# Kernel optimization log

Hardware: AMD Instinct MI355X
Metric: run time of the kernel (lower is better)

Reference implementation:

```python
import jax, jax.numpy as jnp
import numpy as np

N_RAYS = 32768
N_SAMPLES = 1048576
HID = 64
STEP = 0.0005


def _mlp(x, W1, b1, W2, b2, W3, b3):
    h = jax.nn.relu(x @ W1 + b1)
    h = jax.nn.relu(h @ W2 + b2)
    return h @ W3 + b3


def setup_inputs() -> dict:
    key = jax.random.key(0)
    ks = jax.random.split(key, 12)
    rays_o = jax.random.normal(ks[0], (N_RAYS, 3), jnp.float32)
    rays_d = jax.random.normal(ks[1], (N_RAYS, 3), jnp.float32)
    rays_d = rays_d / jnp.linalg.norm(rays_d, axis=-1, keepdims=True)
    t_starts = jax.random.uniform(ks[2], (N_SAMPLES,), jnp.float32, 0.0, 1.5)
    t_ends = t_starts + STEP
    ray_indices = jnp.sort(jax.random.randint(ks[3], (N_SAMPLES,), 0, N_RAYS, jnp.int32))
    def lin(k, fin, fout):
        return jax.random.normal(k, (fin, fout), jnp.float32) / np.sqrt(fin)
    return {
        'rays_o': rays_o, 'rays_d': rays_d,
        't_starts': t_starts, 't_ends': t_ends,
        'ray_indices': ray_indices,
        'W_d1': lin(ks[4], 3, HID), 'b_d1': jnp.zeros((HID,), jnp.float32),
        'W_d2': lin(ks[5], HID, HID), 'b_d2': jnp.zeros((HID,), jnp.float32),
        'W_d3': lin(ks[6], HID, 1), 'b_d3': jnp.zeros((1,), jnp.float32),
        'W_r1': lin(ks[7], 3, HID), 'b_r1': jnp.zeros((HID,), jnp.float32),
        'W_r2': lin(ks[8], HID, HID), 'b_r2': jnp.zeros((HID,), jnp.float32),
        'W_r3': lin(ks[9], HID, 3), 'b_r3': jnp.zeros((3,), jnp.float32),
    }


def reference(rays_o, rays_d, t_starts, t_ends, ray_indices,
              W_d1, b_d1, W_d2, b_d2, W_d3, b_d3,
              W_r1, b_r1, W_r2, b_r2, W_r3, b_r3):
    n_rays = rays_o.shape[0]
    mid = (t_starts + t_ends) * 0.5                      # [S]
    # gather ray origins/dirs per sample, compute positions
    positions = rays_o[ray_indices] + rays_d[ray_indices] * mid[:, None]  # [S,3]
    # density query (NGP decoder stand-in), softplus activation like trunc_exp family
    sigmas = jax.nn.softplus(_mlp(positions, W_d1, b_d1, W_d2, b_d2, W_d3, b_d3))[:, 0]  # [S]
    # render_weight_from_density: segment-wise exclusive cumsum of sigma*dt
    sigma_dt = sigmas * (t_ends - t_starts)              # [S]
    excl_global = jnp.cumsum(sigma_dt) - sigma_dt        # global exclusive cumsum
    per_ray = jax.ops.segment_sum(sigma_dt, ray_indices, num_segments=n_rays)  # [R]
    ray_excl = jnp.cumsum(per_ray) - per_ray             # exclusive cumsum over rays
    within_excl = excl_global - ray_excl[ray_indices]    # exclusive within each ray
    trans = jnp.exp(-within_excl)                        # transmittance
    alphas = 1.0 - jnp.exp(-sigma_dt)
    weights = trans * alphas
    # accumulate_along_rays (scatter-sum over ray_indices)
    opacities = jax.ops.segment_sum(weights, ray_indices, num_segments=n_rays)[:, None]  # [R,1]
    distances = jax.ops.segment_sum(weights * mid, ray_indices, num_segments=n_rays)[:, None]
    # rgb query
    rgbs = jax.nn.sigmoid(_mlp(positions, W_r1, b_r1, W_r2, b_r2, W_r3, b_r3))  # [S,3]
    w_sg = jax.lax.stop_gradient(weights)
    colors = jax.ops.segment_sum(w_sg[:, None] * rgbs, ray_indices, num_segments=n_rays)  # [R,3]
    # eval-mode background composition (nerf.training == False branch)
    rest = jax.lax.stop_gradient(1.0 - opacities)
    distances = distances + 5.0 * rest
    colors = colors + 0.5 * rest
    return colors, distances, opacities
```

## Files before the change

### kernel.cpp

```cpp
#include <hip/hip_runtime.h>
#include <hip/hip_bf16.h>
#include <math.h>

#define N_RAYS   32768
#define N_SAMP   1048576
#define HID      64
#define ITERS    4
#define BLK_HALF 1024
#define BLK_A    (2*BLK_HALF)

typedef short bf8 __attribute__((ext_vector_type(8)));
typedef float f4  __attribute__((ext_vector_type(4)));

union BF8U { bf8 v; unsigned u[4]; };

static __device__ __forceinline__ unsigned bfbits(float x) {
    union { __bf16 h; unsigned short s; } c; c.h = (__bf16)x; return (unsigned)c.s;
}
static __device__ __forceinline__ unsigned pk2(float a, float b) {
#if __has_builtin(__builtin_amdgcn_cvt_pk_bf16_f32)
    return __builtin_bit_cast(unsigned, __builtin_amdgcn_cvt_pk_bf16_f32(a, b));
#else
    return bfbits(a) | (bfbits(b) << 16);
#endif
}
static __device__ __forceinline__ unsigned pk2r(float a, float b) {
    return pk2(fmaxf(a, 0.f), fmaxf(b, 0.f));
}
static __device__ __forceinline__ f4 mfma16(bf8 a, bf8 b, f4 c) {
    return __builtin_amdgcn_mfma_f32_16x16x32_bf16(a, b, c, 0, 0, 0);
}

__global__ __launch_bounds__(256, 2) void pass_a(
    const float* __restrict__ rays_o, const float* __restrict__ rays_d,
    const float* __restrict__ t_starts, const float* __restrict__ t_ends,
    const int*   __restrict__ ray_idx,
    const float* __restrict__ Wd1, const float* __restrict__ bd1,
    const float* __restrict__ Wd2, const float* __restrict__ bd2,
    const float* __restrict__ Wd3, const float* __restrict__ bd3,
    const float* __restrict__ Wr1, const float* __restrict__ br1,
    const float* __restrict__ Wr2, const float* __restrict__ br2,
    const float* __restrict__ Wr3, const float* __restrict__ br3,
    float* __restrict__ ws_sd, float* __restrict__ ws_r,
    float* __restrict__ ws_g,  float* __restrict__ ws_b,
    int* __restrict__ start)
{
    const bool is_rgb = blockIdx.x >= BLK_HALF;
    const int  blk    = is_rgb ? (blockIdx.x - BLK_HALF) : blockIdx.x;
    const int  lane   = threadIdx.x & 63;
    const int  wv     = ((blk << 8) + threadIdx.x) >> 6;
    const int  q      = lane >> 4;
    const int  n      = lane & 15;
    const int  qn     = n >> 2, rn = n & 3;
    const int  rt     = n & 3;

    const float* W1 = is_rgb ? Wr1 : Wd1;  const float* b1 = is_rgb ? br1 : bd1;
    const float* W2 = is_rgb ? Wr2 : Wd2;  const float* b2 = is_rgb ? br2 : bd2;
    const float* W3 = is_rgb ? Wr3 : Wd3;  const float* b3 = is_rgb ? br3 : bd3;
    const int    nc = is_rgb ? 3 : 1;
    const int    ch = is_rgb ? (rt < 3 ? rt : 2) : 0;

    bf8 a1[4];
    #pragma unroll
    for (int t = 0; t < 4; ++t) {
        const int row = 8*qn + 4*(t&1) + rn + 32*(t>>1);
        BF8U f;
        f.u[0] = pk2(W1[row],       W1[HID+row]);
        f.u[1] = pk2(W1[2*HID+row], b1[row]);
        f.u[2] = 0u; f.u[3] = 0u;
        a1[t] = f.v;
    }

    bf8 a2[4][2];
    #pragma unroll
    for (int t = 0; t < 4; ++t) {
        const int row = 8*qn + 4*(t&1) + rn + 32*(t>>1);
        #pragma unroll
        for (int s = 0; s < 2; ++s) {
            BF8U f;
            #pragma unroll
            for (int dw = 0; dw < 4; ++dw) {
                const int k = 8*q + 2*dw + 32*s;
                f.u[dw] = pk2(W2[k*HID+row], W2[(k+1)*HID+row]);
            }
            a2[t][s] = f.v;
        }
    }

    bf8 a3[2];
    #pragma unroll
    for (int s = 0; s < 2; ++s) {
        BF8U f;
        #pragma unroll
        for (int dw = 0; dw < 4; ++dw) {
            const int kg = 32*s + 8*q + 2*dw;
            f.u[dw] = pk2(W3[kg*nc + ch], W3[(kg+1)*nc + ch]);
        }
        a3[s] = f.v;
    }

    f4 bias2[4];
    #pragma unroll
    for (int t = 0; t < 4; ++t) {
        #pragma unroll
        for (int rr = 0; rr < 4; ++rr) {
            const int row = 8*q + 4*(t&1) + rr + 32*(t>>1);
            bias2[t][rr] = b2[row];
        }
    }
    f4 bias3;
    #pragma unroll
    for (int rr = 0; rr < 4; ++rr)
        bias3[rr] = is_rgb ? b3[rr < 3 ? rr : 2] : b3[0];

    const int base0 = wv * (ITERS * 64);

    unsigned p01_[ITERS], p23_[ITERS];
    float    dt_[ITERS];
    #pragma unroll
    for (int it = 0; it < ITERS; ++it) {
        const int smp = base0 + it * 64 + lane;
        const float ts = t_starts[smp], te = t_ends[smp];
        const int   ri = ray_idx[smp];
        const float mid = 0.5f*(ts+te);
        dt_[it] = te - ts;
        const float px = rays_o[3*ri+0] + rays_d[3*ri+0]*mid;
        const float py = rays_o[3*ri+1] + rays_d[3*ri+1]*mid;
        const float pz = rays_o[3*ri+2] + rays_d[3*ri+2]*mid;
        p01_[it] = pk2(px, py);
        p23_[it] = pk2(pz, 1.0f);

        if (!is_rgb) {
            int rp = __shfl_up(ri, 1, 64);
            if (lane == 0) rp = (smp == 0) ? -1 : ray_idx[smp-1];
            for (int rr = rp + 1; rr <= ri; ++rr) start[rr] = smp;
            if (smp == N_SAMP - 1)
                for (int rr = ri + 1; rr <= N_RAYS; ++rr) start[rr] = N_SAMP;
        }
    }

    #pragma unroll
    for (int it = 0; it < ITERS; ++it) {
        const int smp = base0 + it * 64 + lane;

        f4 mine = {0.f, 0.f, 0.f, 0.f};

        #pragma unroll
        for (int u = 0; u < 4; ++u) {
            BF8U xb;
            xb.u[0] = (q == u) ? p01_[it] : 0u;
            xb.u[1] = (q == u) ? p23_[it] : 0u;
            xb.u[2] = 0u; xb.u[3] = 0u;

            const f4 zero = {0.f, 0.f, 0.f, 0.f};
            f4 d1[4];
            #pragma unroll
            for (int t = 0; t < 4; ++t) d1[t] = mfma16(a1[t], xb.v, zero);

            bf8 bf2[2];
            #pragma unroll
            for (int s = 0; s < 2; ++s) {
                BF8U p;
                p.u[0] = pk2r(d1[2*s][0],   d1[2*s][1]);
                p.u[1] = pk2r(d1[2*s][2],   d1[2*s][3]);
                p.u[2] = pk2r(d1[2*s+1][0], d1[2*s+1][1]);
                p.u[3] = pk2r(d1[2*s+1][2], d1[2*s+1][3]);
                bf2[s] = p.v;
            }

            f4 d2[4];
            #pragma unroll
            for (int t = 0; t < 4; ++t) {
                f4 a = bias2[t];
                a = mfma16(a2[t][0], bf2[0], a);
                a = mfma16(a2[t][1], bf2[1], a);
                d2[t] = a;
            }

            bf8 bf3[2];
            #pragma unroll
            for (int s = 0; s < 2; ++s) {
                BF8U p;
                p.u[0] = pk2r(d2[2*s][0],   d2[2*s][1]);
                p.u[1] = pk2r(d2[2*s][2],   d2[2*s][3]);
                p.u[2] = pk2r(d2[2*s+1][0], d2[2*s+1][1]);
                p.u[3] = pk2r(d2[2*s+1][2], d2[2*s+1][3]);
                bf3[s] = p.v;
            }

            f4 c3 = bias3;
            c3 = mfma16(a3[0], bf3[0], c3);
            c3 = mfma16(a3[1], bf3[1], c3);

            if (q == u) mine = c3;
        }

        if (!is_rgb) {
            const float sg = mine[0];
            const float sp = fmaxf(sg, 0.f) + __logf(1.f + __expf(-fabsf(sg)));
            ws_sd[smp] = sp * dt_[it];
        } else {
            ws_r[smp] = __builtin_amdgcn_rcpf(1.f + __expf(-mine[0]));
            ws_g[smp] = __builtin_amdgcn_rcpf(1.f + __expf(-mine[1]));
            ws_b[smp] = __builtin_amdgcn_rcpf(1.f + __expf(-mine[2]));
        }
    }
}

__global__ __launch_bounds__(256) void pass_b(
    const float* __restrict__ t_starts, const float* __restrict__ t_ends,
    const float* __restrict__ ws_sd, const float* __restrict__ ws_r,
    const float* __restrict__ ws_g,  const float* __restrict__ ws_b,
    const int* __restrict__ start, float* __restrict__ out)
{
    const int lane = threadIdx.x & 63;
    const int wv   = (blockIdx.x * blockDim.x + threadIdx.x) >> 6;
    const int half = lane >> 5;
    const int l32  = lane & 31;
    const int r    = 2*wv + half;
    if (r >= N_RAYS) return;

    int s0 = start[r], s1 = start[r+1];
    s0 = min(max(s0, 0), N_SAMP);
    s1 = min(max(s1, s0), N_SAMP);

    float cum = 0.f, opac = 0.f, dist = 0.f, c0 = 0.f, c1 = 0.f, c2 = 0.f;

    for (int base = s0; base < s1; base += 32) {
        int s = base + l32;
        bool ok = s < s1;
        float sd  = ok ? ws_sd[s] : 0.f;
        float vr  = ok ? ws_r[s]  : 0.f;
        float vg  = ok ? ws_g[s]  : 0.f;
        float vb  = ok ? ws_b[s]  : 0.f;
        float mid = ok ? 0.5f*(t_starts[s] + t_ends[s]) : 0.f;

        float x = sd;
        #pragma unroll
        for (int off = 1; off < 32; off <<= 1) {
            float y = __shfl_up(x, off, 32);
            if (l32 >= off) x += y;
        }
        float incl = cum + x;
        float excl = incl - sd;
        float w = __expf(-excl) - __expf(-incl);
        dist += w*mid; c0 += w*vr; c1 += w*vg; c2 += w*vb;

        float tot = __shfl(x, 31, 32);
        opac += __expf(-cum) - __expf(-(cum + tot));
        cum  += tot;
    }

    #pragma unroll
    for (int off = 16; off > 0; off >>= 1) {
        dist += __shfl_xor(dist, off, 32);
        c0   += __shfl_xor(c0,   off, 32);
        c1   += __shfl_xor(c1,   off, 32);
        c2   += __shfl_xor(c2,   off, 32);
    }

    if (l32 == 0) {
        float rest = 1.f - opac;
        out[r*3 + 0] = c0 + 0.5f * rest;
        out[r*3 + 1] = c1 + 0.5f * rest;
        out[r*3 + 2] = c2 + 0.5f * rest;
        out[3*N_RAYS + r] = dist + 5.f * rest;
        out[4*N_RAYS + r] = opac;
    }
}

extern "C" void kernel_launch(void* const* d_in, const int* in_sizes, int n_in,
                              void* d_out, int out_size, void* d_ws, size_t ws_size,
                              hipStream_t stream) {
    const float* rays_o   = (const float*)d_in[0];
    const float* rays_d   = (const float*)d_in[1];
    const float* t_starts = (const float*)d_in[2];
    const float* t_ends   = (const float*)d_in[3];
    const int*   ray_idx  = (const int*)  d_in[4];
    const float* Wd1 = (const float*)d_in[5];  const float* bd1 = (const float*)d_in[6];
    const float* Wd2 = (const float*)d_in[7];  const float* bd2 = (const float*)d_in[8];
    const float* Wd3 = (const float*)d_in[9];  const float* bd3 = (const float*)d_in[10];
    const float* Wr1 = (const float*)d_in[11]; const float* br1 = (const float*)d_in[12];
    const float* Wr2 = (const float*)d_in[13]; const float* br2 = (const float*)d_in[14];
    const float* Wr3 = (const float*)d_in[15]; const float* br3 = (const float*)d_in[16];

    float* ws_sd = (float*)d_ws;
    float* ws_r  = ws_sd + N_SAMP;
    float* ws_g  = ws_r  + N_SAMP;
    float* ws_b  = ws_g  + N_SAMP;
    int*   start = (int*)(ws_b + N_SAMP);
    float* out   = (float*)d_out;

    hipLaunchKernelGGL(pass_a, dim3(BLK_A), dim3(256), 0, stream,
                       rays_o, rays_d, t_starts, t_ends, ray_idx,
                       Wd1, bd1, Wd2, bd2, Wd3, bd3,
                       Wr1, br1, Wr2, br2, Wr3, br3,
                       ws_sd, ws_r, ws_g, ws_b, start);

    hipLaunchKernelGGL(pass_b, dim3((N_RAYS/2 * 64) / 256), dim3(256), 0, stream,
                       t_starts, t_ends, ws_sd, ws_r, ws_g, ws_b, start, out);
}
```

Baseline: 152.5 us.

## Stage MLP weights in shared memory and double samples per wave

Each block now copies the layer weights and biases into shared memory with coalesced float4 loads, then builds its per-lane MFMA fragments from LDS instead of issuing scattered global loads. Samples per wave double and the block count halves, spreading the weight setup over more samples. The launch-bounds occupancy hint is dropped, so register allocation may grow. Fewer blocks and a new barrier could reduce latency hiding.

```diff
diff --git a/kernel.cpp b/kernel.cpp
--- a/kernel.cpp
+++ b/kernel.cpp
@@ -5,8 +5,8 @@
 #define N_RAYS   32768
 #define N_SAMP   1048576
 #define HID      64
-#define ITERS    4
-#define BLK_HALF 1024
+#define ITERS    8
+#define BLK_HALF 512
 #define BLK_A    (2*BLK_HALF)
 
 typedef short bf8 __attribute__((ext_vector_type(8)));
@@ -31,7 +31,7 @@
     return __builtin_amdgcn_mfma_f32_16x16x32_bf16(a, b, c, 0, 0, 0);
 }
 
-__global__ __launch_bounds__(256, 2) void pass_a(
+__global__ __launch_bounds__(256) void pass_a(
     const float* __restrict__ rays_o, const float* __restrict__ rays_d,
     const float* __restrict__ t_starts, const float* __restrict__ t_ends,
     const int*   __restrict__ ray_idx,
@@ -60,13 +60,31 @@
     const int    nc = is_rgb ? 3 : 1;
     const int    ch = is_rgb ? (rt < 3 ? rt : 2) : 0;
 
+    __shared__ float sW1[3*HID];
+    __shared__ float sB1[HID];
+    __shared__ float sW2[HID*HID];
+    __shared__ float sB2[HID];
+    __shared__ float sW3[HID*3];
+    __shared__ float sB3[3];
+    {
+        const int tid = threadIdx.x;
+        #pragma unroll
+        for (int rrd = 0; rrd < 4; ++rrd)
+            ((float4*)sW2)[rrd*256 + tid] = ((const float4*)W2)[rrd*256 + tid];
+        if (tid < 192) sW1[tid] = W1[tid];
+        if (tid < HID) { sB1[tid] = b1[tid]; sB2[tid] = b2[tid]; }
+        if (tid < HID*nc) sW3[tid] = W3[tid];
+        if (tid < nc) sB3[tid] = b3[tid];
+    }
+    __syncthreads();
+
     bf8 a1[4];
     #pragma unroll
     for (int t = 0; t < 4; ++t) {
         const int row = 8*qn + 4*(t&1) + rn + 32*(t>>1);
         BF8U f;
-        f.u[0] = pk2(W1[row],       W1[HID+row]);
-        f.u[1] = pk2(W1[2*HID+row], b1[row]);
+        f.u[0] = pk2(sW1[row],       sW1[HID+row]);
+        f.u[1] = pk2(sW1[2*HID+row], sB1[row]);
         f.u[2] = 0u; f.u[3] = 0u;
         a1[t] = f.v;
     }
@@ -81,7 +99,7 @@
             #pragma unroll
             for (int dw = 0; dw < 4; ++dw) {
                 const int k = 8*q + 2*dw + 32*s;
-                f.u[dw] = pk2(W2[k*HID+row], W2[(k+1)*HID+row]);
+                f.u[dw] = pk2(sW2[k*HID+row], sW2[(k+1)*HID+row]);
             }
             a2[t][s] = f.v;
         }
@@ -94,7 +112,7 @@
         #pragma unroll
         for (int dw = 0; dw < 4; ++dw) {
             const int kg = 32*s + 8*q + 2*dw;
-            f.u[dw] = pk2(W3[kg*nc + ch], W3[(kg+1)*nc + ch]);
+            f.u[dw] = pk2(sW3[kg*nc + ch], sW3[(kg+1)*nc + ch]);
         }
         a3[s] = f.v;
     }
@@ -105,13 +123,13 @@
         #pragma unroll
         for (int rr = 0; rr < 4; ++rr) {
             const int row = 8*q + 4*(t&1) + rr + 32*(t>>1);
-            bias2[t][rr] = b2[row];
+            bias2[t][rr] = sB2[row];
         }
     }
     f4 bias3;
     #pragma unroll
     for (int rr = 0; rr < 4; ++rr)
-        bias3[rr] = is_rgb ? b3[rr < 3 ? rr : 2] : b3[0];
+        bias3[rr] = is_rgb ? sB3[rr < 3 ? rr : 2] : sB3[0];
 
     const int base0 = wv * (ITERS * 64);
 
```

Result: slower. 157.1 us (+3.0%).

## Precompute MFMA weight fragments once and split segment-start computation into its own kernel

Applied to the files above, without the earlier changes.

Adds a single-block prep kernel that packs both MLPs' weights and biases into bf16 MFMA fragment layout in a workspace buffer. Each pass_a wave then loads its fragments with vector loads instead of doing scattered scalar loads and conversions per wave. Segment-start computation moves out of pass_a into a separate kernel, and the launch bounds drop the minimum of two blocks per CU. This removes redundant per-wave setup at the cost of two extra kernel launches and an extra pass over ray_idx.

```diff
diff --git a/kernel.cpp b/kernel.cpp
--- a/kernel.cpp
+++ b/kernel.cpp
@@ -31,87 +31,129 @@
     return __builtin_amdgcn_mfma_f32_16x16x32_bf16(a, b, c, 0, 0, 0);
 }
 
-__global__ __launch_bounds__(256, 2) void pass_a(
-    const float* __restrict__ rays_o, const float* __restrict__ rays_d,
-    const float* __restrict__ t_starts, const float* __restrict__ t_ends,
-    const int*   __restrict__ ray_idx,
+#define FRAG_SLOTS 14
+#define BIAS_SLOTS 5
+
+__global__ __launch_bounds__(128) void prep_frags(
     const float* __restrict__ Wd1, const float* __restrict__ bd1,
     const float* __restrict__ Wd2, const float* __restrict__ bd2,
     const float* __restrict__ Wd3, const float* __restrict__ bd3,
     const float* __restrict__ Wr1, const float* __restrict__ br1,
     const float* __restrict__ Wr2, const float* __restrict__ br2,
     const float* __restrict__ Wr3, const float* __restrict__ br3,
+    uint4* __restrict__ fragbuf, float4* __restrict__ biasbuf)
+{
+    const int tid  = threadIdx.x;
+    if (tid >= 128) return;
+    const int net  = tid >> 6;
+    const int lane = tid & 63;
+    const int q    = lane >> 4;
+    const int n    = lane & 15;
+    const int qn   = n >> 2, rn = n & 3;
+    const int rt   = n & 3;
+
+    const float* W1 = net ? Wr1 : Wd1;  const float* b1 = net ? br1 : bd1;
+    const float* W2 = net ? Wr2 : Wd2;  const float* b2 = net ? br2 : bd2;
+    const float* W3 = net ? Wr3 : Wd3;  const float* b3 = net ? br3 : bd3;
+    const int    nc = net ? 3 : 1;
+    const int    ch = net ? (rt < 3 ? rt : 2) : 0;
+
+    uint4*  fb = fragbuf + net * (FRAG_SLOTS * 64);
+    float4* bb = biasbuf + net * (BIAS_SLOTS * 64);
+
+    for (int t = 0; t < 4; ++t) {
+        const int row = 8*qn + 4*(t&1) + rn + 32*(t>>1);
+        uint4 f;
+        f.x = pk2(W1[row],       W1[HID+row]);
+        f.y = pk2(W1[2*HID+row], b1[row]);
+        f.z = 0u; f.w = 0u;
+        fb[t*64 + lane] = f;
+    }
+    for (int t = 0; t < 4; ++t) {
+        const int row = 8*qn + 4*(t&1) + rn + 32*(t>>1);
+        for (int s = 0; s < 2; ++s) {
+            unsigned u[4];
+            for (int dw = 0; dw < 4; ++dw) {
+                const int k = 8*q + 2*dw + 32*s;
+                u[dw] = pk2(W2[k*HID+row], W2[(k+1)*HID+row]);
+            }
+            fb[(4 + 2*t + s)*64 + lane] = make_uint4(u[0], u[1], u[2], u[3]);
+        }
+    }
+    for (int s = 0; s < 2; ++s) {
+        unsigned u[4];
+        for (int dw = 0; dw < 4; ++dw) {
+            const int kg = 32*s + 8*q + 2*dw;
+            u[dw] = pk2(W3[kg*nc + ch], W3[(kg+1)*nc + ch]);
+        }
+        fb[(12 + s)*64 + lane] = make_uint4(u[0], u[1], u[2], u[3]);
+    }
+    for (int t = 0; t < 4; ++t) {
+        float4 f;
+        f.x = b2[8*q + 4*(t&1) + 0 + 32*(t>>1)];
+        f.y = b2[8*q + 4*(t&1) + 1 + 32*(t>>1)];
+        f.z = b2[8*q + 4*(t&1) + 2 + 32*(t>>1)];
+        f.w = b2[8*q + 4*(t&1) + 3 + 32*(t>>1)];
+        bb[t*64 + lane] = f;
+    }
+    {
+        float4 f;
+        f.x = net ? b3[0] : b3[0];
+        f.y = net ? b3[1] : b3[0];
+        f.z = net ? b3[2] : b3[0];
+        f.w = net ? b3[2] : b3[0];
+        bb[4*64 + lane] = f;
+    }
+}
+
+__global__ __launch_bounds__(256) void seg_starts(
+    const int* __restrict__ ray_idx, int* __restrict__ start)
+{
+    int s = blockIdx.x * blockDim.x + threadIdx.x;
+    if (s >= N_SAMP) return;
+    int b = ray_idx[s];
+    int a = (s == 0) ? -1 : ray_idx[s-1];
+    for (int r = a + 1; r <= b; ++r) start[r] = s;
+    if (s == N_SAMP - 1)
+        for (int r = b + 1; r <= N_RAYS; ++r) start[r] = N_SAMP;
+}
+
+__global__ __launch_bounds__(256) void pass_a(
+    const float* __restrict__ rays_o, const float* __restrict__ rays_d,
+    const float* __restrict__ t_starts, const float* __restrict__ t_ends,
+    const int*   __restrict__ ray_idx,
+    const uint4* __restrict__ fragbuf, const float4* __restrict__ biasbuf,
     float* __restrict__ ws_sd, float* __restrict__ ws_r,
-    float* __restrict__ ws_g,  float* __restrict__ ws_b,
-    int* __restrict__ start)
+    float* __restrict__ ws_g,  float* __restrict__ ws_b)
 {
     const bool is_rgb = blockIdx.x >= BLK_HALF;
     const int  blk    = is_rgb ? (blockIdx.x - BLK_HALF) : blockIdx.x;
     const int  lane   = threadIdx.x & 63;
     const int  wv     = ((blk << 8) + threadIdx.x) >> 6;
     const int  q      = lane >> 4;
-    const int  n      = lane & 15;
-    const int  qn     = n >> 2, rn = n & 3;
-    const int  rt     = n & 3;
-
-    const float* W1 = is_rgb ? Wr1 : Wd1;  const float* b1 = is_rgb ? br1 : bd1;
-    const float* W2 = is_rgb ? Wr2 : Wd2;  const float* b2 = is_rgb ? br2 : bd2;
-    const float* W3 = is_rgb ? Wr3 : Wd3;  const float* b3 = is_rgb ? br3 : bd3;
-    const int    nc = is_rgb ? 3 : 1;
-    const int    ch = is_rgb ? (rt < 3 ? rt : 2) : 0;
+
+    const uint4*  fb = fragbuf + (is_rgb ? FRAG_SLOTS*64 : 0);
+    const float4* bb = biasbuf + (is_rgb ? BIAS_SLOTS*64 : 0);
 
     bf8 a1[4];
     #pragma unroll
-    for (int t = 0; t < 4; ++t) {
-        const int row = 8*qn + 4*(t&1) + rn + 32*(t>>1);
-        BF8U f;
-        f.u[0] = pk2(W1[row],       W1[HID+row]);
-        f.u[1] = pk2(W1[2*HID+row], b1[row]);
-        f.u[2] = 0u; f.u[3] = 0u;
-        a1[t] = f.v;
-    }
-
+    for (int t = 0; t < 4; ++t)
+        a1[t] = __builtin_bit_cast(bf8, fb[t*64 + lane]);
     bf8 a2[4][2];
     #pragma unroll
-    for (int t = 0; t < 4; ++t) {
-        const int row = 8*qn + 4*(t&1) + rn + 32*(t>>1);
+    for (int t = 0; t < 4; ++t)
         #pragma unroll
-        for (int s = 0; s < 2; ++s) {
-            BF8U f;
-            #pragma unroll
-            for (int dw = 0; dw < 4; ++dw) {
-                const int k = 8*q + 2*dw + 32*s;
-                f.u[dw] = pk2(W2[k*HID+row], W2[(k+1)*HID+row]);
-            }
-            a2[t][s] = f.v;
-        }
-    }
-
+        for (int s = 0; s < 2; ++s)
+            a2[t][s] = __builtin_bit_cast(bf8, fb[(4 + 2*t + s)*64 + lane]);
     bf8 a3[2];
     #pragma unroll
-    for (int s = 0; s < 2; ++s) {
-        BF8U f;
-        #pragma unroll
-        for (int dw = 0; dw < 4; ++dw) {
-            const int kg = 32*s + 8*q + 2*dw;
-            f.u[dw] = pk2(W3[kg*nc + ch], W3[(kg+1)*nc + ch]);
-        }
-        a3[s] = f.v;
-    }
-
+    for (int s = 0; s < 2; ++s)
+        a3[s] = __builtin_bit_cast(bf8, fb[(12 + s)*64 + lane]);
     f4 bias2[4];
     #pragma unroll
-    for (int t = 0; t < 4; ++t) {
-        #pragma unroll
-        for (int rr = 0; rr < 4; ++rr) {
-            const int row = 8*q + 4*(t&1) + rr + 32*(t>>1);
-            bias2[t][rr] = b2[row];
-        }
-    }
-    f4 bias3;
-    #pragma unroll
-    for (int rr = 0; rr < 4; ++rr)
-        bias3[rr] = is_rgb ? b3[rr < 3 ? rr : 2] : b3[0];
+    for (int t = 0; t < 4; ++t)
+        bias2[t] = __builtin_bit_cast(f4, bb[t*64 + lane]);
+    f4 bias3 = __builtin_bit_cast(f4, bb[4*64 + lane]);
 
     const int base0 = wv * (ITERS * 64);
 
@@ -129,14 +171,6 @@
         const float pz = rays_o[3*ri+2] + rays_d[3*ri+2]*mid;
         p01_[it] = pk2(px, py);
         p23_[it] = pk2(pz, 1.0f);
-
-        if (!is_rgb) {
-            int rp = __shfl_up(ri, 1, 64);
-            if (lane == 0) rp = (smp == 0) ? -1 : ray_idx[smp-1];
-            for (int rr = rp + 1; rr <= ri; ++rr) start[rr] = smp;
-            if (smp == N_SAMP - 1)
-                for (int rr = ri + 1; rr <= N_RAYS; ++rr) start[rr] = N_SAMP;
-        }
     }
 
     #pragma unroll
@@ -288,14 +322,22 @@
     float* ws_r  = ws_sd + N_SAMP;
     float* ws_g  = ws_r  + N_SAMP;
     float* ws_b  = ws_g  + N_SAMP;
-    int*   start = (int*)(ws_b + N_SAMP);
-    float* out   = (float*)d_out;
+    char*  p     = (char*)(ws_b + N_SAMP);
+    int*    start   = (int*)p;
+    uint4*  fragbuf = (uint4*)(p + ((N_RAYS+1)*4 + 255 & ~255));
+    float4* biasbuf = (float4*)(fragbuf + 2*FRAG_SLOTS*64);
+    float*  out     = (float*)d_out;
+
+    hipLaunchKernelGGL(prep_frags, dim3(1), dim3(128), 0, stream,
+                       Wd1, bd1, Wd2, bd2, Wd3, bd3,
+                       Wr1, br1, Wr2, br2, Wr3, br3, fragbuf, biasbuf);
+
+    hipLaunchKernelGGL(seg_starts, dim3((N_SAMP + 255)/256), dim3(256), 0, stream,
+                       ray_idx, start);
 
     hipLaunchKernelGGL(pass_a, dim3(BLK_A), dim3(256), 0, stream,
                        rays_o, rays_d, t_starts, t_ends, ray_idx,
-                       Wd1, bd1, Wd2, bd2, Wd3, bd3,
-                       Wr1, br1, Wr2, br2, Wr3, br3,
-                       ws_sd, ws_r, ws_g, ws_b, start);
+                       fragbuf, biasbuf, ws_sd, ws_r, ws_g, ws_b);
 
     hipLaunchKernelGGL(pass_b, dim3((N_RAYS/2 * 64) / 256), dim3(256), 0, stream,
                        t_starts, t_ends, ws_sd, ws_r, ws_g, ws_b, start, out);
```

After: 155.1 us. No clear change (+1.7%).
